# Performance work log

Hardware: AMD Instinct MI355X
Metric: run time of the kernel (lower is better)

## Reference

```python
import jax, jax.numpy as jnp
import numpy as np
from jax import lax

# --- block geometry (matches init_kwargs) ---
B = 8
DIM = 192
HEADS = 6
KEY_DIM = DIM // HEADS  # 32, attn_ratio=1 so d == key_dim and dh == DIM
HX, WX = 32, 32         # search region
HZ, WZ = 16, 16         # template region
T = 1                   # template_number
L = HX * WX + T * HZ * WZ  # 1280 tokens
MLP_HIDDEN = int(DIM * 4.0)
BN_EPS = 1e-5


def _build_bias_idx():
    """Replicates Attention.__init__ global_att=True bias-index construction.
    Unique-offset ids may be permuted vs torch dict-insertion order, which is an
    equivalent reparameterization of the (randomly initialized) bias table."""
    g = np.stack(np.meshgrid(np.arange(HX), np.arange(WX), indexing='ij'), -1).reshape(-1, 2)
    pts = [g]
    for i in range(T):
        r = np.arange(HX + HZ * i, WX + WZ * (i + 1))
        g2 = np.stack(np.meshgrid(r, r, indexing='ij'), -1).reshape(-1, 2)
        pts.append(g2)
    p = np.concatenate(pts, 0)                      # (L, 2)
    off = np.abs(p[:, None, :] - p[None, :, :])     # (L, L, 2)
    key = off[:, :, 0].astype(np.int64) * 4096 + off[:, :, 1]
    uniq, inv = np.unique(key, return_inverse=True)
    return inv.reshape(L, L).astype(np.int32), int(len(uniq))


def setup_inputs() -> dict:
    key = jax.random.key(0)
    ks = jax.random.split(key, 16)
    idx_np, n_off = _build_bias_idx()
    s = 0.02
    return {
        'xz': jax.random.normal(ks[0], (B, L, DIM), jnp.float32),
        'bias_idx': jnp.asarray(idx_np),
        'ln1_g': jnp.ones((DIM,), jnp.float32),
        'ln1_b': jnp.zeros((DIM,), jnp.float32),
        'wqkv': jax.random.normal(ks[1], (DIM, 3 * DIM), jnp.float32) * s,
        'bqkv': jnp.zeros((3 * DIM,), jnp.float32),
        'wproj': jax.random.normal(ks[2], (DIM, DIM), jnp.float32) * s,
        'bproj': jnp.zeros((DIM,), jnp.float32),
        'bias_table': jax.random.normal(ks[3], (HEADS, n_off), jnp.float32) * 0.1,
        'conv_w': jax.random.normal(ks[4], (3, 3, 1, DIM), jnp.float32) * 0.1,  # depthwise HWIO
        'bn_scale': jnp.ones((DIM,), jnp.float32) + jax.random.normal(ks[5], (DIM,), jnp.float32) * 0.01,
        'bn_bias': jax.random.normal(ks[6], (DIM,), jnp.float32) * 0.01,
        'ln2_g': jnp.ones((DIM,), jnp.float32),
        'ln2_b': jnp.zeros((DIM,), jnp.float32),
        'w1': jax.random.normal(ks[7], (DIM, MLP_HIDDEN), jnp.float32) * s,
        'b1': jnp.zeros((MLP_HIDDEN,), jnp.float32),
        'w2': jax.random.normal(ks[8], (MLP_HIDDEN, DIM), jnp.float32) * s,
        'b2': jnp.zeros((DIM,), jnp.float32),
    }


def _layernorm(x, g, b, eps=1e-5):
    mu = jnp.mean(x, -1, keepdims=True)
    var = jnp.mean(jnp.square(x - mu), -1, keepdims=True)
    return (x - mu) * lax.rsqrt(var + eps) * g + b


def reference(xz, bias_idx, ln1_g, ln1_b, wqkv, bqkv, wproj, bproj, bias_table,
              conv_w, bn_scale, bn_bias, ln2_g, ln2_b, w1, b1, w2, b2):
    Bn, N, D = xz.shape
    scale = KEY_DIM ** -0.5
    # --- Attention (LeViT-style with gathered relative-position bias) ---
    h = _layernorm(xz, ln1_g, ln1_b)
    qkv = (h @ wqkv + bqkv).reshape(Bn, N, HEADS, 3 * KEY_DIM)
    q, k, v = jnp.split(qkv, 3, axis=3)            # each (B, N, H, key_dim)
    bias = bias_table[:, bias_idx]                  # (H, N, N) gather
    attn = jnp.einsum('bnhd,bmhd->bhnm', q, k) * scale + bias
    attn = jax.nn.softmax(attn, axis=-1)
    o = jnp.einsum('bhnm,bmhd->bnhd', attn, v).reshape(Bn, N, D)
    xm = xz + o @ wproj + bproj
    # --- depthwise local conv (Conv2d_BN, BN folded to scale/bias) per segment ---
    segs = []
    start = 0
    for (Hh, Ww) in [(HX, WX)] + [(HZ, WZ)] * T:
        xc = xm[:, start:start + Hh * Ww, :].reshape(Bn, Hh, Ww, D)
        xc = lax.conv_general_dilated(
            xc, conv_w, window_strides=(1, 1), padding='SAME',
            dimension_numbers=('NHWC', 'HWIO', 'NHWC'), feature_group_count=D)
        xc = xc * bn_scale + bn_bias
        segs.append(xc.reshape(Bn, Hh * Ww, D))
        start += Hh * Ww
    xm = jnp.concatenate(segs, axis=1)
    # --- MLP with pre-LN (exact GELU, matching nn.GELU default) ---
    m = _layernorm(xm, ln2_g, ln2_b)
    m = jax.nn.gelu(m @ w1 + b1, approximate=False) @ w2 + b2
    return xm + m
```

## Files before the change

### kernel.cpp

```cpp
#include <hip/hip_runtime.h>
#include <hip/hip_bf16.h>

#define BATCH 8
#define LTOK 1280
#define DIMC 192
#define HEADS 6
#define KD 32
#define HID 768
#define NROWS (BATCH*LTOK)

typedef short s16x8 __attribute__((ext_vector_type(8)));
typedef float f32x4 __attribute__((ext_vector_type(4)));
typedef unsigned short u16;

#define QS (0.17677669529663687f * 1.4426950408889634f)
#define L2E 1.4426950408889634f

__device__ __forceinline__ u16 f2bf(float x) {
    unsigned u = __float_as_uint(x);
    u = (u + 0x7FFFu + ((u >> 16) & 1u)) >> 16;
    return (u16)u;
}
__device__ __forceinline__ float bflo(unsigned u) { return __uint_as_float(u << 16); }
__device__ __forceinline__ float bfhi(unsigned u) { return __uint_as_float(u & 0xffff0000u); }
__device__ __forceinline__ float fexp2(float x) { float r; asm("v_exp_f32 %0, %1" : "=v"(r) : "v"(x)); return r; }
__device__ __forceinline__ float frcp(float x)  { float r; asm("v_rcp_f32 %0, %1" : "=v"(r) : "v"(x)); return r; }

__global__ __launch_bounds__(256) void pre_kernel(const float* w0, const float* w1,
                                                  const float* w2, const float* w3,
                                                  u16* o0, u16* o1, u16* o2, u16* o3,
                                                  const int* __restrict__ bidx,
                                                  const float* __restrict__ btab,
                                                  int n_off, u16* __restrict__ bmp,
                                                  const float* __restrict__ xz,
                                                  const float* __restrict__ ln1g,
                                                  const float* __restrict__ ln1b,
                                                  u16* __restrict__ hbuf) {
    __shared__ float s[16][17];
    int f = blockIdx.x;
    if (f >= 11328) {
        int row = (f - 11328) * 4 + (threadIdx.x >> 6);
        int lane = threadIdx.x & 63;
        const float* xr = xz + (size_t)row * DIMC;
        float v0 = xr[lane], v1 = xr[lane + 64], v2 = xr[lane + 128];
        float sm = v0 + v1 + v2;
        float ss = v0 * v0 + v1 * v1 + v2 * v2;
        #pragma unroll
        for (int off = 32; off; off >>= 1) {
            sm += __shfl_xor(sm, off);
            ss += __shfl_xor(ss, off);
        }
        float mu  = sm * (1.0f / DIMC);
        float var = ss * (1.0f / DIMC) - mu * mu;
        float inv = rsqrtf(var + 1e-5f);
        u16* yr = hbuf + (size_t)row * DIMC;
        yr[lane]       = f2bf((v0 - mu) * inv * ln1g[lane]       + ln1b[lane]);
        yr[lane + 64]  = f2bf((v1 - mu) * inv * ln1g[lane + 64]  + ln1b[lane + 64]);
        yr[lane + 128] = f2bf((v2 - mu) * inv * ln1g[lane + 128] + ln1b[lane + 128]);
        return;
    }
    if (f >= 1728) {
        int fb = f - 1728;
        int qt = fb / 120;
        int rem = fb - qt * 120;
        int T = rem / 6, h = rem - (rem / 6) * 6;
        int tid = threadIdx.x;
        int half = tid >> 7, L = (tid >> 1) & 63, j4 = (tid & 1) * 4;
        int n = qt * 16 + (L & 15);
        int m = T * 64 + half * 32 + ((L >> 4) << 3) + j4;
        int4 iv = *(const int4*)(bidx + (size_t)n * LTOK + m);
        const float* tab = btab + (size_t)h * n_off;
        ushort4 o;
        o.x = f2bf(tab[iv.x] * L2E);
        o.y = f2bf(tab[iv.y] * L2E);
        o.z = f2bf(tab[iv.z] * L2E);
        o.w = f2bf(tab[iv.w] * L2E);
        *(ushort4*)(bmp + (size_t)(h * 80 + qt) * 20480 + T * 1024 + tid * 4) = o;
        return;
    }
    const float* in; u16* out; int K, N, tn, tk;
    if (f < 432)       { in = w0; out = o0; K = 192; N = 576; int r = f;        tn = r % 36; tk = r / 36; }
    else if (f < 576)  { in = w1; out = o1; K = 192; N = 192; int r = f - 432;  tn = r % 12; tk = r / 12; }
    else if (f < 1152) { in = w2; out = o2; K = 192; N = 768; int r = f - 576;  tn = r % 48; tk = r / 48; }
    else               { in = w3; out = o3; K = 768; N = 192; int r = f - 1152; tn = r % 12; tk = r / 12; }
    int tx = threadIdx.x & 15, ty = threadIdx.x >> 4;
    s[ty][tx] = in[(size_t)(tk * 16 + ty) * N + tn * 16 + tx];
    __syncthreads();
    out[(size_t)(tn * 16 + ty) * K + tk * 16 + tx] = f2bf(s[tx][ty]);
}

template<int ACT, int RES, int OBF, int QKV, int K, int MTILE>
__global__ __launch_bounds__(256) void gemm_mfma(const u16* __restrict__ A,
                                                 const u16* __restrict__ Wt,
                                                 const float* __restrict__ bias,
                                                 const float* __restrict__ R,
                                                 void* __restrict__ Cp,
                                                 u16* __restrict__ qb,
                                                 u16* __restrict__ kp,
                                                 u16* __restrict__ vp,
                                                 int N) {
    constexpr int SUB = MTILE / 64;
    int tid = threadIdx.x;
    int L = tid & 63, w = tid >> 6;
    int r = L & 15, g = L >> 4;
    int m0 = blockIdx.y * MTILE + w * (16 * SUB);
    int n0 = blockIdx.x * 64;

    f32x4 acc[SUB][4] = {};
    const u16* Ab = A + (size_t)(m0 + r) * K + g * 8;
    const u16* Wb = Wt + (size_t)(n0 + r) * K + g * 8;
    #pragma unroll 6
    for (int k0 = 0; k0 < K; k0 += 32) {
        s16x8 af[SUB];
        #pragma unroll
        for (int mi = 0; mi < SUB; ++mi)
            af[mi] = *(const s16x8*)(Ab + (size_t)mi * 16 * K + k0);
        #pragma unroll
        for (int nn = 0; nn < 4; ++nn) {
            s16x8 bf = *(const s16x8*)(Wb + (size_t)nn * 16 * K + k0);
            #pragma unroll
            for (int mi = 0; mi < SUB; ++mi)
                acc[mi][nn] = __builtin_amdgcn_mfma_f32_16x16x32_bf16(af[mi], bf, acc[mi][nn], 0, 0, 0);
        }
    }

    #pragma unroll
    for (int mi = 0; mi < SUB; ++mi)
    #pragma unroll
    for (int nn = 0; nn < 4; ++nn) {
        int cb = n0 + nn * 16;
        #pragma unroll
        for (int i = 0; i < 4; ++i) {
            int row = m0 + mi * 16 + g * 4 + i;
            float v = acc[mi][nn][i] + bias[cb + r];
            if (QKV) {
                int h  = cb / 96, c0 = cb % 96;
                int reg = c0 >> 5;
                if (reg == 0) {
                    v *= QS;
                    qb[(size_t)row * DIMC + h * 32 + (c0 & 31) + r] = f2bf(v);
                } else {
                    int b_ = row / LTOK, t = row - b_ * LTOK;
                    int T = t >> 5, it = t & 31;
                    int d = (c0 & 31) + r;
                    if (reg == 1) {
                        int which = (it >> 2) & 1;
                        int ik = ((it >> 3) << 2) | (it & 3);
                        int Lk = ((d >> 3) << 4) + ik;
                        kp[((size_t)(b_ * HEADS + h) * 40 + T) * 1024 + which * 512 + Lk * 8 + (d & 7)] = f2bf(v);
                    } else {
                        int Lv = ((it >> 3) << 4) + (d & 15);
                        vp[((size_t)(b_ * HEADS + h) * 40 + T) * 1024 + (d >> 4) * 512 + Lv * 8 + (it & 7)] = f2bf(v);
                    }
                }
            } else {
                if (ACT == 1) {
                    float u = v;
                    float y = 0.7978845608028654f * (u + 0.044715f * u * u * u);
                    float e2 = fexp2(y * 2.885390081777927f);
                    v = u - u * frcp(e2 + 1.0f);
                }
                if (RES) v += R[(size_t)row * N + cb + r];
                if (OBF) ((u16*)Cp)[(size_t)row * N + cb + r] = f2bf(v);
                else     ((float*)Cp)[(size_t)row * N + cb + r] = v;
            }
        }
    }
}

__global__ __launch_bounds__(256) void attn_mfma(const u16* __restrict__ qb,
                                                 const u16* __restrict__ kp,
                                                 const u16* __restrict__ vp,
                                                 const u16* __restrict__ bmp,
                                                 u16* __restrict__ ob) {
    __shared__ __align__(16) u16 kvs[2][2][2048];
    int tid = threadIdx.x;
    int L = tid & 63, w = tid >> 6;
    int r = L & 15, g = L >> 4;
    int L8 = L * 8;

    int bid = blockIdx.x;
    int work = (bid & 7) * 120 + (bid >> 3);
    int b  = work & 7;
    int hq = work >> 3;
    int qt = (hq % 20) * 4 + w;
    int h  = hq / 20;

    s16x8 qf = *(const s16x8*)(qb + (size_t)(b * LTOK + qt * 16 + r) * DIMC + h * 32 + g * 8);

    int skv = w >> 1, half = w & 1;
    const u16* gs = (skv ? vp : kp) + (size_t)(b * HEADS + h) * 40 * 1024 + L8;
    u16* dst0 = &kvs[0][skv][half * 1024 + L8];
    u16* dst1 = &kvs[1][skv][half * 1024 + L8];

    const u16* bmr = bmp + (size_t)(h * 80 + qt) * 20480 + L8;

    f32x4 acc0 = {0.f, 0.f, 0.f, 0.f}, acc1 = {0.f, 0.f, 0.f, 0.f};
    float lsum = 0.f;

    {
        int4 pA = *(const int4*)(gs + half * 1024);
        int4 pB = *(const int4*)(gs + half * 1024 + 512);
        *(int4*)dst0 = pA;
        *(int4*)(dst0 + 512) = pB;
    }
    int4 cb0 = *(const int4*)(bmr);
    int4 cb1 = *(const int4*)(bmr + 512);
    __syncthreads();

    f32x4 s0, s1, s2, s3;
    {
        const u16* kb = &kvs[0][0][0];
        f32x4 z0, z1, z2, z3;
        z0[0] = bflo(cb0.x); z0[1] = bfhi(cb0.x); z0[2] = bflo(cb0.y); z0[3] = bfhi(cb0.y);
        z1[0] = bflo(cb0.z); z1[1] = bfhi(cb0.z); z1[2] = bflo(cb0.w); z1[3] = bfhi(cb0.w);
        z2[0] = bflo(cb1.x); z2[1] = bfhi(cb1.x); z2[2] = bflo(cb1.y); z2[3] = bfhi(cb1.y);
        z3[0] = bflo(cb1.z); z3[1] = bfhi(cb1.z); z3[2] = bflo(cb1.w); z3[3] = bfhi(cb1.w);
        s16x8 kf0 = *(const s16x8*)(kb + L8);
        s16x8 kf1 = *(const s16x8*)(kb + 512 + L8);
        s16x8 kf2 = *(const s16x8*)(kb + 1024 + L8);
        s16x8 kf3 = *(const s16x8*)(kb + 1536 + L8);
        s0 = __builtin_amdgcn_mfma_f32_16x16x32_bf16(kf0, qf, z0, 0, 0, 0);
        s1 = __builtin_amdgcn_mfma_f32_16x16x32_bf16(kf1, qf, z1, 0, 0, 0);
        s2 = __builtin_amdgcn_mfma_f32_16x16x32_bf16(kf2, qf, z2, 0, 0, 0);
        s3 = __builtin_amdgcn_mfma_f32_16x16x32_bf16(kf3, qf, z3, 0, 0, 0);
    }

    #pragma unroll 1
    for (int T = 0; T < 20; ++T) {
        int4 nA, nB, nb0, nb1;
        if (T < 19) {
            nA  = *(const int4*)(gs + (size_t)(2 * T + 2 + half) * 1024);
            nB  = *(const int4*)(gs + (size_t)(2 * T + 2 + half) * 1024 + 512);
            nb0 = *(const int4*)(bmr + (size_t)(T + 1) * 1024);
            nb1 = *(const int4*)(bmr + (size_t)(T + 1) * 1024 + 512);
        }
        __builtin_amdgcn_s_setprio(1);
        float p[16];
        #pragma unroll
        for (int j = 0; j < 4; ++j) {
            p[j]      = fexp2(s0[j]);
            p[4 + j]  = fexp2(s1[j]);
            p[8 + j]  = fexp2(s2[j]);
            p[12 + j] = fexp2(s3[j]);
        }
        float t0 = ((p[0] + p[1]) + (p[2] + p[3])) + ((p[4] + p[5]) + (p[6] + p[7]));
        float t1 = ((p[8] + p[9]) + (p[10] + p[11])) + ((p[12] + p[13]) + (p[14] + p[15]));
        lsum += t0 + t1;
        union { unsigned u[4]; s16x8 v; } pa, pb;
        #pragma unroll
        for (int j = 0; j < 4; ++j) {
            asm("v_cvt_pk_bf16_f32 %0, %1, %2" : "=v"(pa.u[j]) : "v"(p[2 * j]), "v"(p[2 * j + 1]));
            asm("v_cvt_pk_bf16_f32 %0, %1, %2" : "=v"(pb.u[j]) : "v"(p[8 + 2 * j]), "v"(p[9 + 2 * j]));
        }
        const u16* vb = &kvs[T & 1][1][0];
        s16x8 v0 = *(const s16x8*)(vb + L8);
        s16x8 v1 = *(const s16x8*)(vb + 512 + L8);
        s16x8 v2 = *(const s16x8*)(vb + 1024 + L8);
        s16x8 v3 = *(const s16x8*)(vb + 1536 + L8);
        acc0 = __builtin_amdgcn_mfma_f32_16x16x32_bf16(pa.v, v0, acc0, 0, 0, 0);
        acc1 = __builtin_amdgcn_mfma_f32_16x16x32_bf16(pa.v, v1, acc1, 0, 0, 0);
        acc0 = __builtin_amdgcn_mfma_f32_16x16x32_bf16(pb.v, v2, acc0, 0, 0, 0);
        acc1 = __builtin_amdgcn_mfma_f32_16x16x32_bf16(pb.v, v3, acc1, 0, 0, 0);
        __builtin_amdgcn_s_setprio(0);

        if (T < 19) {
            u16* d = (T & 1) ? dst0 : dst1;
            *(int4*)d = nA;
            *(int4*)(d + 512) = nB;
        }
        __syncthreads();
        if (T < 19) {
            const u16* kb = &kvs[(T + 1) & 1][0][0];
            f32x4 z0, z1, z2, z3;
            z0[0] = bflo(nb0.x); z0[1] = bfhi(nb0.x); z0[2] = bflo(nb0.y); z0[3] = bfhi(nb0.y);
            z1[0] = bflo(nb0.z); z1[1] = bfhi(nb0.z); z1[2] = bflo(nb0.w); z1[3] = bfhi(nb0.w);
            z2[0] = bflo(nb1.x); z2[1] = bfhi(nb1.x); z2[2] = bflo(nb1.y); z2[3] = bfhi(nb1.y);
            z3[0] = bflo(nb1.z); z3[1] = bfhi(nb1.z); z3[2] = bflo(nb1.w); z3[3] = bfhi(nb1.w);
            s16x8 kf0 = *(const s16x8*)(kb + L8);
            s16x8 kf1 = *(const s16x8*)(kb + 512 + L8);
            s16x8 kf2 = *(const s16x8*)(kb + 1024 + L8);
            s16x8 kf3 = *(const s16x8*)(kb + 1536 + L8);
            __builtin_amdgcn_s_setprio(1);
            s0 = __builtin_amdgcn_mfma_f32_16x16x32_bf16(kf0, qf, z0, 0, 0, 0);
            s1 = __builtin_amdgcn_mfma_f32_16x16x32_bf16(kf1, qf, z1, 0, 0, 0);
            s2 = __builtin_amdgcn_mfma_f32_16x16x32_bf16(kf2, qf, z2, 0, 0, 0);
            s3 = __builtin_amdgcn_mfma_f32_16x16x32_bf16(kf3, qf, z3, 0, 0, 0);
            __builtin_amdgcn_s_setprio(0);
        }
    }

    float lr = lsum;
    lr += __shfl_xor(lr, 16);
    lr += __shfl_xor(lr, 32);
    #pragma unroll
    for (int i = 0; i < 4; ++i) {
        float linv = frcp(__shfl(lr, 4 * g + i));
        size_t orow = (size_t)(b * LTOK + qt * 16 + 4 * g + i) * DIMC + h * 32 + r;
        ob[orow]      = f2bf(acc0[i] * linv);
        ob[orow + 16] = f2bf(acc1[i] * linv);
    }
}

__global__ __launch_bounds__(256) void conv_ln_kernel(const float* __restrict__ xm,
                                                      const float* __restrict__ w,
                                                      const float* __restrict__ scale,
                                                      const float* __restrict__ bias,
                                                      const float* __restrict__ g2,
                                                      const float* __restrict__ b2,
                                                      float* __restrict__ xm2,
                                                      u16* __restrict__ y) {
    int row = blockIdx.x * 4 + (threadIdx.x >> 6);
    int lane = threadIdx.x & 63;
    int b = row / LTOK, t = row - b * LTOK;
    int H, W, base, y0, x0;
    if (t < 1024) { H = 32; W = 32; base = 0;    y0 = t >> 5;            x0 = t & 31; }
    else          { H = 16; W = 16; base = 1024; int tt = t - 1024; y0 = tt >> 4; x0 = tt & 15; }
    float a0 = 0.f, a1 = 0.f, a2 = 0.f;
    #pragma unroll
    for (int ky = 0; ky < 3; ++ky) {
        int yy = y0 + ky - 1;
        if (yy < 0 || yy >= H) continue;
        #pragma unroll
        for (int kx = 0; kx < 3; ++kx) {
            int xx = x0 + kx - 1;
            if (xx < 0 || xx >= W) continue;
            const float* xr = xm + (size_t)(b * LTOK + base + yy * W + xx) * DIMC;
            const float* wr = w + (ky * 3 + kx) * DIMC;
            a0 += wr[lane]       * xr[lane];
            a1 += wr[lane + 64]  * xr[lane + 64];
            a2 += wr[lane + 128] * xr[lane + 128];
        }
    }
    float v0 = a0 * scale[lane]       + bias[lane];
    float v1 = a1 * scale[lane + 64]  + bias[lane + 64];
    float v2 = a2 * scale[lane + 128] + bias[lane + 128];
    float* xr2 = xm2 + (size_t)row * DIMC;
    xr2[lane] = v0; xr2[lane + 64] = v1; xr2[lane + 128] = v2;
    float s = v0 + v1 + v2;
    float ss = v0 * v0 + v1 * v1 + v2 * v2;
    #pragma unroll
    for (int off = 32; off; off >>= 1) {
        s  += __shfl_xor(s, off);
        ss += __shfl_xor(ss, off);
    }
    float mu  = s * (1.0f / DIMC);
    float var = ss * (1.0f / DIMC) - mu * mu;
    float inv = rsqrtf(var + 1e-5f);
    u16* yr = y + (size_t)row * DIMC;
    yr[lane]       = f2bf((v0 - mu) * inv * g2[lane]       + b2[lane]);
    yr[lane + 64]  = f2bf((v1 - mu) * inv * g2[lane + 64]  + b2[lane + 64]);
    yr[lane + 128] = f2bf((v2 - mu) * inv * g2[lane + 128] + b2[lane + 128]);
}

extern "C" void kernel_launch(void* const* d_in, const int* in_sizes, int n_in,
                              void* d_out, int out_size, void* d_ws, size_t ws_size,
                              hipStream_t stream) {
    const float* xz       = (const float*)d_in[0];
    const int*   bidx     = (const int*)  d_in[1];
    const float* ln1_g    = (const float*)d_in[2];
    const float* ln1_b    = (const float*)d_in[3];
    const float* wqkv     = (const float*)d_in[4];
    const float* bqkv     = (const float*)d_in[5];
    const float* wproj    = (const float*)d_in[6];
    const float* bproj    = (const float*)d_in[7];
    const float* btab     = (const float*)d_in[8];
    const float* conv_w   = (const float*)d_in[9];
    const float* bn_scale = (const float*)d_in[10];
    const float* bn_bias  = (const float*)d_in[11];
    const float* ln2_g    = (const float*)d_in[12];
    const float* ln2_b    = (const float*)d_in[13];
    const float* w1       = (const float*)d_in[14];
    const float* b1       = (const float*)d_in[15];
    const float* w2       = (const float*)d_in[16];
    const float* b2       = (const float*)d_in[17];
    int n_off = in_sizes[8] / HEADS;
    float* out = (float*)d_out;

    char* wsb = (char*)d_ws;
    u16*  hbuf   = (u16*)(wsb + 0);
    u16*  ob     = (u16*)(wsb + 0);
    u16*  wqkvT  = (u16*)(wsb + 3932160);
    u16*  wprojT = (u16*)(wsb + 4153344);
    u16*  w1T    = (u16*)(wsb + 4227072);
    u16*  w2T    = (u16*)(wsb + 4521984);
    u16*  bmp    = (u16*)(wsb + 4816896);
    u16*  hid    = (u16*)(wsb + 4816896);
    u16*  kp     = (u16*)(wsb + 24477696);
    u16*  vp     = (u16*)(wsb + 28409856);
    float* xm2   = (float*)(wsb + 24477696);
    u16*  qb     = (u16*)(wsb + 32342016);
    float* xm    = (float*)(wsb + 32342016);

    pre_kernel<<<13888, 256, 0, stream>>>(
        wqkv, wproj, w1, w2, wqkvT, wprojT, w1T, w2T, bidx, btab, n_off, bmp,
        xz, ln1_g, ln1_b, hbuf);
    gemm_mfma<0,0,0,1,DIMC,256><<<dim3(576 / 64, NROWS / 256), 256, 0, stream>>>(
        hbuf, wqkvT, bqkv, nullptr, nullptr, qb, kp, vp, 3 * DIMC);
    attn_mfma<<<960, 256, 0, stream>>>(qb, kp, vp, bmp, ob);
    gemm_mfma<0,1,0,0,DIMC,128><<<dim3(DIMC / 64, NROWS / 128), 256, 0, stream>>>(
        ob, wprojT, bproj, xz, xm, nullptr, nullptr, nullptr, DIMC);
    conv_ln_kernel<<<NROWS / 4, 256, 0, stream>>>(
        xm, conv_w, bn_scale, bn_bias, ln2_g, ln2_b, xm2, hbuf);
    gemm_mfma<1,0,1,0,DIMC,256><<<dim3(HID / 64, NROWS / 256), 256, 0, stream>>>(
        hbuf, w1T, b1, nullptr, hid, nullptr, nullptr, nullptr, HID);
    gemm_mfma<0,1,0,0,HID,128><<<dim3(DIMC / 64, NROWS / 128), 256, 0, stream>>>(
        hid, w2T, b2, xm2, out, nullptr, nullptr, nullptr, DIMC);
}
```

Baseline: 124.2 us.

## Move bias-map gather and weight transposes into the QKV GEMM launch

Splits the old pre-kernel. The first kernel now does only the QKV weight transpose and LN1. The relative-position bias gather and the other weight transposes move into the QKV GEMM launch as extra blocks, so this memory-bound work runs alongside the matrix math instead of before it. The QKV GEMM becomes a dedicated kernel, and the QKV epilogue branch is removed from the generic GEMM template. Block ordering matters: the GEMM blocks come first and the long gather tail follows, which could cause imbalance.

```diff
diff --git a/kernel.cpp b/kernel.cpp
--- a/kernel.cpp
+++ b/kernel.cpp
@@ -26,20 +26,16 @@
 __device__ __forceinline__ float fexp2(float x) { float r; asm("v_exp_f32 %0, %1" : "=v"(r) : "v"(x)); return r; }
 __device__ __forceinline__ float frcp(float x)  { float r; asm("v_rcp_f32 %0, %1" : "=v"(r) : "v"(x)); return r; }
 
-__global__ __launch_bounds__(256) void pre_kernel(const float* w0, const float* w1,
-                                                  const float* w2, const float* w3,
-                                                  u16* o0, u16* o1, u16* o2, u16* o3,
-                                                  const int* __restrict__ bidx,
-                                                  const float* __restrict__ btab,
-                                                  int n_off, u16* __restrict__ bmp,
-                                                  const float* __restrict__ xz,
-                                                  const float* __restrict__ ln1g,
-                                                  const float* __restrict__ ln1b,
-                                                  u16* __restrict__ hbuf) {
+__global__ __launch_bounds__(256) void pre_a(const float* __restrict__ w0,
+                                             u16* __restrict__ o0,
+                                             const float* __restrict__ xz,
+                                             const float* __restrict__ ln1g,
+                                             const float* __restrict__ ln1b,
+                                             u16* __restrict__ hbuf) {
     __shared__ float s[16][17];
     int f = blockIdx.x;
-    if (f >= 11328) {
-        int row = (f - 11328) * 4 + (threadIdx.x >> 6);
+    if (f >= 432) {
+        int row = (f - 432) * 4 + (threadIdx.x >> 6);
         int lane = threadIdx.x & 63;
         const float* xr = xz + (size_t)row * DIMC;
         float v0 = xr[lane], v1 = xr[lane + 64], v2 = xr[lane + 128];
@@ -59,8 +55,44 @@
         yr[lane + 128] = f2bf((v2 - mu) * inv * ln1g[lane + 128] + ln1b[lane + 128]);
         return;
     }
-    if (f >= 1728) {
-        int fb = f - 1728;
+    int tn = f % 36, tk = f / 36;
+    int tx = threadIdx.x & 15, ty = threadIdx.x >> 4;
+    s[ty][tx] = w0[(size_t)(tk * 16 + ty) * 576 + tn * 16 + tx];
+    __syncthreads();
+    o0[(size_t)(tn * 16 + ty) * 192 + tk * 16 + tx] = f2bf(s[tx][ty]);
+}
+
+__global__ __launch_bounds__(256) void qkv_mega(const u16* __restrict__ A,
+                                                const u16* __restrict__ Wt,
+                                                const float* __restrict__ bias,
+                                                u16* __restrict__ qb,
+                                                u16* __restrict__ kp,
+                                                u16* __restrict__ vp,
+                                                const int* __restrict__ bidx,
+                                                const float* __restrict__ btab,
+                                                int n_off, u16* __restrict__ bmp,
+                                                const float* __restrict__ wp,
+                                                const float* __restrict__ wf1,
+                                                const float* __restrict__ wf2,
+                                                u16* __restrict__ op,
+                                                u16* __restrict__ of1,
+                                                u16* __restrict__ of2) {
+    int bid = blockIdx.x;
+    if (bid >= 9960) {
+        __shared__ float s[16][17];
+        int f2 = bid - 9960;
+        const float* in; u16* out; int K, N, tn, tk;
+        if (f2 < 144)      { in = wp;  out = op;  K = 192; N = 192; tn = f2 % 12; tk = f2 / 12; }
+        else if (f2 < 720) { in = wf1; out = of1; K = 192; N = 768; int q = f2 - 144; tn = q % 48; tk = q / 48; }
+        else               { in = wf2; out = of2; K = 768; N = 192; int q = f2 - 720; tn = q % 12; tk = q / 12; }
+        int tx = threadIdx.x & 15, ty = threadIdx.x >> 4;
+        s[ty][tx] = in[(size_t)(tk * 16 + ty) * N + tn * 16 + tx];
+        __syncthreads();
+        out[(size_t)(tn * 16 + ty) * K + tk * 16 + tx] = f2bf(s[tx][ty]);
+        return;
+    }
+    if (bid >= 360) {
+        int fb = bid - 360;
         int qt = fb / 120;
         int rem = fb - qt * 120;
         int T = rem / 6, h = rem - (rem / 6) * 6;
@@ -78,26 +110,68 @@
         *(ushort4*)(bmp + (size_t)(h * 80 + qt) * 20480 + T * 1024 + tid * 4) = o;
         return;
     }
-    const float* in; u16* out; int K, N, tn, tk;
-    if (f < 432)       { in = w0; out = o0; K = 192; N = 576; int r = f;        tn = r % 36; tk = r / 36; }
-    else if (f < 576)  { in = w1; out = o1; K = 192; N = 192; int r = f - 432;  tn = r % 12; tk = r / 12; }
-    else if (f < 1152) { in = w2; out = o2; K = 192; N = 768; int r = f - 576;  tn = r % 48; tk = r / 48; }
-    else               { in = w3; out = o3; K = 768; N = 192; int r = f - 1152; tn = r % 12; tk = r / 12; }
-    int tx = threadIdx.x & 15, ty = threadIdx.x >> 4;
-    s[ty][tx] = in[(size_t)(tk * 16 + ty) * N + tn * 16 + tx];
-    __syncthreads();
-    out[(size_t)(tn * 16 + ty) * K + tk * 16 + tx] = f2bf(s[tx][ty]);
-}
-
-template<int ACT, int RES, int OBF, int QKV, int K, int MTILE>
+    int bx = bid % 9, by = bid / 9;
+    int tid = threadIdx.x;
+    int L = tid & 63, w = tid >> 6;
+    int r = L & 15, g = L >> 4;
+    int m0 = by * 256 + w * 64;
+    int n0 = bx * 64;
+
+    f32x4 acc[4][4] = {};
+    const u16* Ab = A + (size_t)(m0 + r) * 192 + g * 8;
+    const u16* Wb = Wt + (size_t)(n0 + r) * 192 + g * 8;
+    #pragma unroll 6
+    for (int k0 = 0; k0 < 192; k0 += 32) {
+        s16x8 af[4];
+        #pragma unroll
+        for (int mi = 0; mi < 4; ++mi)
+            af[mi] = *(const s16x8*)(Ab + (size_t)mi * 16 * 192 + k0);
+        #pragma unroll
+        for (int nn = 0; nn < 4; ++nn) {
+            s16x8 bf = *(const s16x8*)(Wb + (size_t)nn * 16 * 192 + k0);
+            #pragma unroll
+            for (int mi = 0; mi < 4; ++mi)
+                acc[mi][nn] = __builtin_amdgcn_mfma_f32_16x16x32_bf16(af[mi], bf, acc[mi][nn], 0, 0, 0);
+        }
+    }
+    #pragma unroll
+    for (int mi = 0; mi < 4; ++mi)
+    #pragma unroll
+    for (int nn = 0; nn < 4; ++nn) {
+        int cb = n0 + nn * 16;
+        int h  = cb / 96, c0 = cb % 96;
+        int reg = c0 >> 5;
+        #pragma unroll
+        for (int i = 0; i < 4; ++i) {
+            int row = m0 + mi * 16 + g * 4 + i;
+            float v = acc[mi][nn][i] + bias[cb + r];
+            if (reg == 0) {
+                v *= QS;
+                qb[(size_t)row * DIMC + h * 32 + (c0 & 31) + r] = f2bf(v);
+            } else {
+                int b_ = row / LTOK, t = row - b_ * LTOK;
+                int T = t >> 5, it = t & 31;
+                int d = (c0 & 31) + r;
+                if (reg == 1) {
+                    int which = (it >> 2) & 1;
+                    int ik = ((it >> 3) << 2) | (it & 3);
+                    int Lk = ((d >> 3) << 4) + ik;
+                    kp[((size_t)(b_ * HEADS + h) * 40 + T) * 1024 + which * 512 + Lk * 8 + (d & 7)] = f2bf(v);
+                } else {
+                    int Lv = ((it >> 3) << 4) + (d & 15);
+                    vp[((size_t)(b_ * HEADS + h) * 40 + T) * 1024 + (d >> 4) * 512 + Lv * 8 + (it & 7)] = f2bf(v);
+                }
+            }
+        }
+    }
+}
+
+template<int ACT, int RES, int OBF, int K, int MTILE>
 __global__ __launch_bounds__(256) void gemm_mfma(const u16* __restrict__ A,
                                                  const u16* __restrict__ Wt,
                                                  const float* __restrict__ bias,
                                                  const float* __restrict__ R,
                                                  void* __restrict__ Cp,
-                                                 u16* __restrict__ qb,
-                                                 u16* __restrict__ kp,
-                                                 u16* __restrict__ vp,
                                                  int N) {
     constexpr int SUB = MTILE / 64;
     int tid = threadIdx.x;
@@ -133,37 +207,15 @@
         for (int i = 0; i < 4; ++i) {
             int row = m0 + mi * 16 + g * 4 + i;
             float v = acc[mi][nn][i] + bias[cb + r];
-            if (QKV) {
-                int h  = cb / 96, c0 = cb % 96;
-                int reg = c0 >> 5;
-                if (reg == 0) {
-                    v *= QS;
-                    qb[(size_t)row * DIMC + h * 32 + (c0 & 31) + r] = f2bf(v);
-                } else {
-                    int b_ = row / LTOK, t = row - b_ * LTOK;
-                    int T = t >> 5, it = t & 31;
-                    int d = (c0 & 31) + r;
-                    if (reg == 1) {
-                        int which = (it >> 2) & 1;
-                        int ik = ((it >> 3) << 2) | (it & 3);
-                        int Lk = ((d >> 3) << 4) + ik;
-                        kp[((size_t)(b_ * HEADS + h) * 40 + T) * 1024 + which * 512 + Lk * 8 + (d & 7)] = f2bf(v);
-                    } else {
-                        int Lv = ((it >> 3) << 4) + (d & 15);
-                        vp[((size_t)(b_ * HEADS + h) * 40 + T) * 1024 + (d >> 4) * 512 + Lv * 8 + (it & 7)] = f2bf(v);
-                    }
-                }
-            } else {
-                if (ACT == 1) {
-                    float u = v;
-                    float y = 0.7978845608028654f * (u + 0.044715f * u * u * u);
-                    float e2 = fexp2(y * 2.885390081777927f);
-                    v = u - u * frcp(e2 + 1.0f);
-                }
-                if (RES) v += R[(size_t)row * N + cb + r];
-                if (OBF) ((u16*)Cp)[(size_t)row * N + cb + r] = f2bf(v);
-                else     ((float*)Cp)[(size_t)row * N + cb + r] = v;
+            if (ACT == 1) {
+                float u = v;
+                float y = 0.7978845608028654f * (u + 0.044715f * u * u * u);
+                float e2 = fexp2(y * 2.885390081777927f);
+                v = u - u * frcp(e2 + 1.0f);
             }
+            if (RES) v += R[(size_t)row * N + cb + r];
+            if (OBF) ((u16*)Cp)[(size_t)row * N + cb + r] = f2bf(v);
+            else     ((float*)Cp)[(size_t)row * N + cb + r] = v;
         }
     }
 }
@@ -392,18 +444,18 @@
     u16*  qb     = (u16*)(wsb + 32342016);
     float* xm    = (float*)(wsb + 32342016);
 
-    pre_kernel<<<13888, 256, 0, stream>>>(
-        wqkv, wproj, w1, w2, wqkvT, wprojT, w1T, w2T, bidx, btab, n_off, bmp,
-        xz, ln1_g, ln1_b, hbuf);
-    gemm_mfma<0,0,0,1,DIMC,256><<<dim3(576 / 64, NROWS / 256), 256, 0, stream>>>(
-        hbuf, wqkvT, bqkv, nullptr, nullptr, qb, kp, vp, 3 * DIMC);
+    pre_a<<<432 + NROWS / 4, 256, 0, stream>>>(wqkv, wqkvT, xz, ln1_g, ln1_b, hbuf);
+    qkv_mega<<<11256, 256, 0, stream>>>(
+        hbuf, wqkvT, bqkv, qb, kp, vp,
+        bidx, btab, n_off, bmp,
+        wproj, w1, w2, wprojT, w1T, w2T);
     attn_mfma<<<960, 256, 0, stream>>>(qb, kp, vp, bmp, ob);
-    gemm_mfma<0,1,0,0,DIMC,128><<<dim3(DIMC / 64, NROWS / 128), 256, 0, stream>>>(
-        ob, wprojT, bproj, xz, xm, nullptr, nullptr, nullptr, DIMC);
+    gemm_mfma<0,1,0,DIMC,128><<<dim3(DIMC / 64, NROWS / 128), 256, 0, stream>>>(
+        ob, wprojT, bproj, xz, xm, DIMC);
     conv_ln_kernel<<<NROWS / 4, 256, 0, stream>>>(
         xm, conv_w, bn_scale, bn_bias, ln2_g, ln2_b, xm2, hbuf);
-    gemm_mfma<1,0,1,0,DIMC,256><<<dim3(HID / 64, NROWS / 256), 256, 0, stream>>>(
-        hbuf, w1T, b1, nullptr, hid, nullptr, nullptr, nullptr, HID);
-    gemm_mfma<0,1,0,0,HID,128><<<dim3(DIMC / 64, NROWS / 128), 256, 0, stream>>>(
-        hid, w2T, b2, xm2, out, nullptr, nullptr, nullptr, DIMC);
-}
+    gemm_mfma<1,0,1,DIMC,256><<<dim3(HID / 64, NROWS / 256), 256, 0, stream>>>(
+        hbuf, w1T, b1, nullptr, hid, HID);
+    gemm_mfma<0,1,0,HID,128><<<dim3(DIMC / 64, NROWS / 128), 256, 0, stream>>>(
+        hid, w2T, b2, xm2, out, DIMC);
+}
```

Result: faster. 120.5 us (-2.9%).
